# Performance work log

Measured on AMD Instinct MI355X. Metric: run time of the kernel, lower is better.

The kernel has to match this reference:

```python
import jax, jax.numpy as jnp
import numpy as np

HIDDEN = 1024
NUM_EXPERTS = 8
TOP_K = 2
CAPACITY_FACTOR = 1.5
B, S = 2, 2048


def setup_inputs() -> dict:
    key = jax.random.key(0)
    k0, k1, k2 = jax.random.split(key, 3)
    sc1 = 1.0 / np.sqrt(HIDDEN)
    return {
        "hidden_states": jax.random.normal(k0, (B, S, HIDDEN), dtype=jnp.float32),
        "w1": jax.random.uniform(k1, (HIDDEN, HIDDEN), jnp.float32, -sc1, sc1),
        "b1": jnp.zeros((HIDDEN,), jnp.float32),
        "w2": jax.random.uniform(k2, (NUM_EXPERTS, HIDDEN), jnp.float32, -sc1, sc1),
        "b2": jnp.zeros((NUM_EXPERTS,), jnp.float32),
    }


def reference(hidden_states, w1, b1, w2, b2):
    bsz, seq, hid = hidden_states.shape
    # router MLP: Linear -> ReLU -> Linear
    h = jax.nn.relu(jnp.einsum("bsh,oh->bso", hidden_states, w1) + b1)
    router_logits = jnp.einsum("bsh,eh->bse", h, w2) + b2  # [B,S,E]
    router_probs = jax.nn.softmax(router_logits, axis=-1)

    top_k_probs, top_k_indices = jax.lax.top_k(router_probs, TOP_K)  # [B,S,K]
    top_k_probs = top_k_probs / jnp.sum(top_k_probs, axis=-1, keepdims=True)

    capacity = int(bsz * seq * CAPACITY_FACTOR * TOP_K / NUM_EXPERTS)  # static

    # Original writes ONLY capacity slot 0 for each selected expert.
    onehot = jax.nn.one_hot(top_k_indices, NUM_EXPERTS, dtype=router_probs.dtype)  # [B,S,K,E]
    slot0_dispatch = jnp.sum(onehot, axis=-2)                      # [B,S,E] (top-k experts distinct)
    slot0_combine = jnp.einsum("bske,bsk->bse", onehot, top_k_probs)

    dispatch_tensor = jnp.zeros((bsz, seq, NUM_EXPERTS, capacity), router_probs.dtype)
    dispatch_tensor = dispatch_tensor.at[..., 0].set(slot0_dispatch)
    combine_tensor = jnp.zeros((bsz, seq, NUM_EXPERTS, capacity), router_probs.dtype)
    combine_tensor = combine_tensor.at[..., 0].set(slot0_combine)

    router_prob_per_expert = jnp.mean(router_probs, axis=(0, 1))  # [E]
    aux_loss = jnp.sum(router_prob_per_expert * jnp.log(router_prob_per_expert * NUM_EXPERTS + 1e-9))
    return dispatch_tensor, combine_tensor, router_probs, aux_loss
```

## Files before the change

kernel.cpp:

```cpp
#include <hip/hip_runtime.h>
#include <hip/hip_bf16.h>
#include <math.h>

#define HID  1024
#define NEXP 8
#define CAP  1536
#define NTOK 4096

#define DISP_OFF 0ull
#define COMB_OFF 50331648ull
#define RP_OFF   100663296ull
#define AUX_OFF  100696064ull

typedef float f32x4 __attribute__((ext_vector_type(4)));
typedef short s16x8 __attribute__((ext_vector_type(8)));
typedef unsigned short u16;

#define PART_F 524288
#define OXH_F  526400
#define OXM_F  2623552
#define OWH_F  4720704
#define OWM_F  5244992

__device__ __forceinline__ void cvt8(const float4 v0, const float4 v1, s16x8& hi, s16x8& mi)
{
    float f[8] = {v0.x, v0.y, v0.z, v0.w, v1.x, v1.y, v1.z, v1.w};
#pragma unroll
    for (int i = 0; i < 8; ++i) {
        __hip_bfloat16 h = __float2bfloat16(f[i]);
        float fh = __bfloat162float(h);
        __hip_bfloat16 m = __float2bfloat16(f[i] - fh);
        hi[i] = (short)__builtin_bit_cast(unsigned short, h);
        mi[i] = (short)__builtin_bit_cast(unsigned short, m);
    }
}

__device__ __forceinline__ void gload16(const void* g, void* l)
{
    __builtin_amdgcn_global_load_lds(
        (const __attribute__((address_space(1))) unsigned int*)g,
        (__attribute__((address_space(3))) unsigned int*)l, 16, 0, 0);
}

__global__ __launch_bounds__(256) void prep_kernel(
    const float* __restrict__ X, const float* __restrict__ W1, float* __restrict__ ws)
{
    const int g = blockIdx.x * 256 + threadIdx.x;
    const float* src;
    u16 *dh, *dm;
    int idx;
    if (g < 524288) { src = X;  dh = (u16*)(ws + OXH_F); dm = (u16*)(ws + OXM_F); idx = g; }
    else            { src = W1; dh = (u16*)(ws + OWH_F); dm = (u16*)(ws + OWM_F); idx = g - 524288; }
    float4 v0 = *(const float4*)(src + (size_t)idx * 8);
    float4 v1 = *(const float4*)(src + (size_t)idx * 8 + 4);
    s16x8 hi, mi;
    cvt8(v0, v1, hi, mi);
    *(s16x8*)(dh + (size_t)idx * 8) = hi;
    *(s16x8*)(dm + (size_t)idx * 8) = mi;
}

__global__ void fused_kernel(
    const float* __restrict__ B1, const float* __restrict__ W2,
    float* __restrict__ ws, float* __restrict__ out)
{
    __shared__ s16x8 L[2][4][128][4];
    const int tid = threadIdx.x, bid = blockIdx.x;

    if (bid >= 256) {
        const int zid = bid - 256;
        f32x4* p = (f32x4*)out + (size_t)zid * 98304 + tid;
        f32x4 z = (f32x4)0.0f;
#pragma unroll 8
        for (int i = 0; i < 384; ++i) { __builtin_nontemporal_store(z, p); p += 256; }
        return;
    }

    const int n0 = (bid & 7) * 128;
    const int m0 = (bid >> 3) * 128;
    const int wave = tid >> 6, lane = tid & 63;
    const int wr = wave >> 1, wc = wave & 1;
    const int fr = lane & 15, fk = lane >> 4;

    const u16* XH = (const u16*)(ws + OXH_F);
    const u16* XM = (const u16*)(ws + OXM_F);
    const u16* WH = (const u16*)(ws + OWH_F);
    const u16* WM = (const u16*)(ws + OWM_F);

    const int sr4 = lane >> 2;
    const int cg  = (lane & 3) ^ (sr4 & 3);
    const u16* sb = (wave & 2)
        ? (((wave & 1) ? WM : WH) + (size_t)(n0 + sr4) * HID + cg * 8)
        : (((wave & 1) ? XM : XH) + (size_t)(m0 + sr4) * HID + cg * 8);
    char* db = (char*)&L[0][wave][0][0];

    f32x4 acc[4][4];
#pragma unroll
    for (int i = 0; i < 4; ++i)
#pragma unroll
        for (int j = 0; j < 4; ++j) acc[i][j] = (f32x4)0.0f;

#pragma unroll
    for (int i = 0; i < 8; ++i)
        gload16(sb + (size_t)i * 16 * HID, db + i * 1024);
    __syncthreads();

    for (int kk = 0; kk < 32; ++kk) {
        const int b = kk & 1;
        if (kk + 1 < 32) {
            const u16* s = sb + (kk + 1) * 32;
            char* d = db + (b ^ 1) * 32768;
#pragma unroll
            for (int i = 0; i < 8; ++i)
                gload16(s + (size_t)i * 16 * HID, d + i * 1024);
        }

        const s16x8 (*LAh)[4] = L[b][0];
        const s16x8 (*LAm)[4] = L[b][1];
        const s16x8 (*LBh)[4] = L[b][2];
        const s16x8 (*LBm)[4] = L[b][3];
        const int sl = fk ^ (fr & 3);
        s16x8 bh[4], bm[4];
#pragma unroll
        for (int j = 0; j < 4; ++j) {
            const int rb = wc * 64 + j * 16 + fr;
            bh[j] = LBh[rb][sl];
            bm[j] = LBm[rb][sl];
        }
#pragma unroll
        for (int i = 0; i < 4; ++i) {
            const int ra = wr * 64 + i * 16 + fr;
            s16x8 ah = LAh[ra][sl];
            s16x8 am = LAm[ra][sl];
#pragma unroll
            for (int j = 0; j < 4; ++j) {
                acc[i][j] = __builtin_amdgcn_mfma_f32_16x16x32_bf16(ah, bh[j], acc[i][j], 0, 0, 0);
                acc[i][j] = __builtin_amdgcn_mfma_f32_16x16x32_bf16(ah, bm[j], acc[i][j], 0, 0, 0);
                acc[i][j] = __builtin_amdgcn_mfma_f32_16x16x32_bf16(am, bh[j], acc[i][j], 0, 0, 0);
            }
        }
        __syncthreads();
    }

    const int colbase = n0 + wc * 64 + fr;
#pragma unroll
    for (int j = 0; j < 4; ++j) {
        const float bj = B1[colbase + j * 16];
#pragma unroll
        for (int i = 0; i < 4; ++i)
#pragma unroll
            for (int r = 0; r < 4; ++r)
                acc[i][j][r] = fmaxf(acc[i][j][r] + bj, 0.f);
    }

    const int slice = (bid & 7) * 2 + wc;
    float* pbase = ws + ((size_t)slice * NTOK + (m0 + wr * 64 + fk * 4)) * NEXP;
#pragma unroll
    for (int e = 0; e < 8; ++e) {
        const float w20 = W2[e * HID + colbase];
        const float w21 = W2[e * HID + colbase + 16];
        const float w22 = W2[e * HID + colbase + 32];
        const float w23 = W2[e * HID + colbase + 48];
        float pe[16];
#pragma unroll
        for (int i = 0; i < 4; ++i)
#pragma unroll
            for (int r = 0; r < 4; ++r)
                pe[i * 4 + r] = acc[i][0][r] * w20 + acc[i][1][r] * w21 +
                                acc[i][2][r] * w22 + acc[i][3][r] * w23;
#pragma unroll
        for (int m = 1; m <= 8; m <<= 1)
#pragma unroll
            for (int q = 0; q < 16; ++q)
                pe[q] += __shfl_xor(pe[q], m, 64);
        if (fr == 0) {
#pragma unroll
            for (int i = 0; i < 4; ++i)
#pragma unroll
                for (int r = 0; r < 4; ++r)
                    pbase[(size_t)(i * 16 + r) * NEXP + e] = pe[i * 4 + r];
        }
    }
}

__global__ __launch_bounds__(256) void router2_kernel(
    const float* __restrict__ ws, const float* __restrict__ B2, float* __restrict__ out)
{
    const int t = blockIdx.x * 256 + threadIdx.x;
    float lg[8];
#pragma unroll
    for (int e = 0; e < 8; ++e) lg[e] = 0.f;
#pragma unroll
    for (int s = 0; s < 16; ++s) {
        const float* p = ws + ((size_t)s * NTOK + t) * NEXP;
        f32x4 v0 = *(const f32x4*)p;
        f32x4 v1 = *(const f32x4*)(p + 4);
        lg[0] += v0.x; lg[1] += v0.y; lg[2] += v0.z; lg[3] += v0.w;
        lg[4] += v1.x; lg[5] += v1.y; lg[6] += v1.z; lg[7] += v1.w;
    }
#pragma unroll
    for (int e = 0; e < 8; ++e) lg[e] += B2[e];

    float mx = lg[0];
#pragma unroll
    for (int e = 1; e < 8; ++e) mx = fmaxf(mx, lg[e]);
    float pr[8], s = 0.f;
#pragma unroll
    for (int e = 0; e < 8; ++e) { pr[e] = expf(lg[e] - mx); s += pr[e]; }
    const float inv = 1.f / s;
#pragma unroll
    for (int e = 0; e < 8; ++e) pr[e] *= inv;

    int e1 = 0; float p1 = pr[0];
#pragma unroll
    for (int e = 1; e < 8; ++e) if (pr[e] > p1) { p1 = pr[e]; e1 = e; }
    int e2 = -1; float p2 = -1.f;
#pragma unroll
    for (int e = 0; e < 8; ++e) if (e != e1 && pr[e] > p2) { p2 = pr[e]; e2 = e; }

    const float invs = 1.f / (p1 + p2);
    float* rp = out + RP_OFF + (size_t)t * NEXP;
    f32x4 o0 = {pr[0], pr[1], pr[2], pr[3]};
    f32x4 o1 = {pr[4], pr[5], pr[6], pr[7]};
    *(f32x4*)rp = o0; *(f32x4*)(rp + 4) = o1;

    const size_t base = (size_t)t * NEXP;
    out[DISP_OFF + (base + e1) * CAP] = 1.0f;
    out[DISP_OFF + (base + e2) * CAP] = 1.0f;
    out[COMB_OFF + (base + e1) * CAP] = p1 * invs;
    out[COMB_OFF + (base + e2) * CAP] = p2 * invs;
}

__global__ __launch_bounds__(256) void aux_kernel(float* __restrict__ out)
{
    __shared__ float sm[NEXP][257];
    const int tid = threadIdx.x;
    float s[NEXP];
#pragma unroll
    for (int e = 0; e < 8; ++e) s[e] = 0.f;
    const float* rp = out + RP_OFF;
    for (int t = tid; t < NTOK; t += 256) {
        f32x4 v0 = *(const f32x4*)&rp[(size_t)t * NEXP];
        f32x4 v1 = *(const f32x4*)&rp[(size_t)t * NEXP + 4];
        s[0] += v0.x; s[1] += v0.y; s[2] += v0.z; s[3] += v0.w;
        s[4] += v1.x; s[5] += v1.y; s[6] += v1.z; s[7] += v1.w;
    }
#pragma unroll
    for (int e = 0; e < 8; ++e) sm[e][tid] = s[e];
    __syncthreads();
    for (int st = 128; st > 0; st >>= 1) {
        if (tid < st) {
#pragma unroll
            for (int e = 0; e < 8; ++e) sm[e][tid] += sm[e][tid + st];
        }
        __syncthreads();
    }
    if (tid == 0) {
        float loss = 0.f;
#pragma unroll
        for (int e = 0; e < 8; ++e) {
            float m = sm[e][0] * (1.0f / NTOK);
            loss += m * logf(m * (float)NEXP + 1e-9f);
        }
        out[AUX_OFF] = loss;
    }
}

extern "C" void kernel_launch(void* const* d_in, const int* in_sizes, int n_in,
                              void* d_out, int out_size, void* d_ws, size_t ws_size,
                              hipStream_t stream)
{
    const float* x  = (const float*)d_in[0];
    const float* w1 = (const float*)d_in[1];
    const float* b1 = (const float*)d_in[2];
    const float* w2 = (const float*)d_in[3];
    const float* b2 = (const float*)d_in[4];
    float* out = (float*)d_out;
    float* ws  = (float*)d_ws;

    prep_kernel<<<2560, 256, 0, stream>>>(x, w1, ws);
    fused_kernel<<<512, 256, 0, stream>>>(b1, w2, ws, out);
    router2_kernel<<<16, 256, 0, stream>>>(ws, b2, out);
    aux_kernel<<<1, 256, 0, stream>>>(out);
}
```

Measured before the change: 442.7 us.

## Interleave output zero-fill stores into GEMM k-loop with 512-thread blocks

Removes the separate zero-fill blocks and has each GEMM block issue nontemporal zero stores for its slice of the output inside every k-iteration, overlapping the large memory-bound fill with MFMA compute. Blocks grow to 512 threads (8 waves), each wave owning a 32x64 sub-tile, so per-wave accumulator registers halve and each wave loads half as many LDS rows. The cost is more store traffic competing with the global-to-LDS loads, and only 256 blocks in the grid.

```diff
diff --git a/kernel.cpp b/kernel.cpp
--- a/kernel.cpp
+++ b/kernel.cpp
@@ -59,21 +59,12 @@
     *(s16x8*)(dm + (size_t)idx * 8) = mi;
 }
 
-__global__ void fused_kernel(
+__global__ __launch_bounds__(512) void fused_kernel(
     const float* __restrict__ B1, const float* __restrict__ W2,
     float* __restrict__ ws, float* __restrict__ out)
 {
     __shared__ s16x8 L[2][4][128][4];
     const int tid = threadIdx.x, bid = blockIdx.x;
-
-    if (bid >= 256) {
-        const int zid = bid - 256;
-        f32x4* p = (f32x4*)out + (size_t)zid * 98304 + tid;
-        f32x4 z = (f32x4)0.0f;
-#pragma unroll 8
-        for (int i = 0; i < 384; ++i) { __builtin_nontemporal_store(z, p); p += 256; }
-        return;
-    }
 
     const int n0 = (bid & 7) * 128;
     const int m0 = (bid >> 3) * 128;
@@ -86,32 +77,41 @@
     const u16* WH = (const u16*)(ws + OWH_F);
     const u16* WM = (const u16*)(ws + OWM_F);
 
+    f32x4* zp = (f32x4*)out + (size_t)bid * 98304 + tid;
+    const f32x4 zv = (f32x4)0.0f;
+
+    const int st = wave >> 1, hf = wave & 1;
     const int sr4 = lane >> 2;
     const int cg  = (lane & 3) ^ (sr4 & 3);
-    const u16* sb = (wave & 2)
-        ? (((wave & 1) ? WM : WH) + (size_t)(n0 + sr4) * HID + cg * 8)
-        : (((wave & 1) ? XM : XH) + (size_t)(m0 + sr4) * HID + cg * 8);
-    char* db = (char*)&L[0][wave][0][0];
-
-    f32x4 acc[4][4];
+    const u16* sb = (st >= 2)
+        ? (((st == 3) ? WM : WH) + (size_t)(n0 + hf * 64 + sr4) * HID + cg * 8)
+        : (((st == 1) ? XM : XH) + (size_t)(m0 + hf * 64 + sr4) * HID + cg * 8);
+    char* db0 = (char*)&L[0][st][0][0] + hf * 4096;
+
+    f32x4 acc[2][4];
+#pragma unroll
+    for (int i = 0; i < 2; ++i)
+#pragma unroll
+        for (int j = 0; j < 4; ++j) acc[i][j] = (f32x4)0.0f;
+
 #pragma unroll
     for (int i = 0; i < 4; ++i)
-#pragma unroll
-        for (int j = 0; j < 4; ++j) acc[i][j] = (f32x4)0.0f;
-
-#pragma unroll
-    for (int i = 0; i < 8; ++i)
-        gload16(sb + (size_t)i * 16 * HID, db + i * 1024);
+        gload16(sb + (size_t)i * 16 * HID, db0 + i * 1024);
     __syncthreads();
 
     for (int kk = 0; kk < 32; ++kk) {
         const int b = kk & 1;
         if (kk + 1 < 32) {
-            const u16* s = sb + (kk + 1) * 32;
-            char* d = db + (b ^ 1) * 32768;
-#pragma unroll
-            for (int i = 0; i < 8; ++i)
+            const u16* s = sb + (size_t)(kk + 1) * 32;
+            char* d = db0 + (b ^ 1) * 32768;
+#pragma unroll
+            for (int i = 0; i < 4; ++i)
                 gload16(s + (size_t)i * 16 * HID, d + i * 1024);
+        }
+#pragma unroll
+        for (int i2 = 0; i2 < 6; ++i2) {
+            __builtin_nontemporal_store(zv, zp);
+            zp += 512;
         }
 
         const s16x8 (*LAh)[4] = L[b][0];
@@ -127,8 +127,8 @@
             bm[j] = LBm[rb][sl];
         }
 #pragma unroll
-        for (int i = 0; i < 4; ++i) {
-            const int ra = wr * 64 + i * 16 + fr;
+        for (int i = 0; i < 2; ++i) {
+            const int ra = wr * 32 + i * 16 + fr;
             s16x8 ah = LAh[ra][sl];
             s16x8 am = LAm[ra][sl];
 #pragma unroll
@@ -146,23 +146,23 @@
     for (int j = 0; j < 4; ++j) {
         const float bj = B1[colbase + j * 16];
 #pragma unroll
-        for (int i = 0; i < 4; ++i)
+        for (int i = 0; i < 2; ++i)
 #pragma unroll
             for (int r = 0; r < 4; ++r)
                 acc[i][j][r] = fmaxf(acc[i][j][r] + bj, 0.f);
     }
 
     const int slice = (bid & 7) * 2 + wc;
-    float* pbase = ws + ((size_t)slice * NTOK + (m0 + wr * 64 + fk * 4)) * NEXP;
+    float* pbase = ws + ((size_t)slice * NTOK + (m0 + wr * 32 + fk * 4)) * NEXP;
 #pragma unroll
     for (int e = 0; e < 8; ++e) {
         const float w20 = W2[e * HID + colbase];
         const float w21 = W2[e * HID + colbase + 16];
         const float w22 = W2[e * HID + colbase + 32];
         const float w23 = W2[e * HID + colbase + 48];
-        float pe[16];
-#pragma unroll
-        for (int i = 0; i < 4; ++i)
+        float pe[8];
+#pragma unroll
+        for (int i = 0; i < 2; ++i)
 #pragma unroll
             for (int r = 0; r < 4; ++r)
                 pe[i * 4 + r] = acc[i][0][r] * w20 + acc[i][1][r] * w21 +
@@ -170,11 +170,11 @@
 #pragma unroll
         for (int m = 1; m <= 8; m <<= 1)
 #pragma unroll
-            for (int q = 0; q < 16; ++q)
+            for (int q = 0; q < 8; ++q)
                 pe[q] += __shfl_xor(pe[q], m, 64);
         if (fr == 0) {
 #pragma unroll
-            for (int i = 0; i < 4; ++i)
+            for (int i = 0; i < 2; ++i)
 #pragma unroll
                 for (int r = 0; r < 4; ++r)
                     pbase[(size_t)(i * 16 + r) * NEXP + e] = pe[i * 4 + r];
@@ -278,7 +278,7 @@
     float* ws  = (float*)d_ws;
 
     prep_kernel<<<2560, 256, 0, stream>>>(x, w1, ws);
-    fused_kernel<<<512, 256, 0, stream>>>(b1, w2, ws, out);
+    fused_kernel<<<256, 512, 0, stream>>>(b1, w2, ws, out);
     router2_kernel<<<16, 256, 0, stream>>>(ws, b2, out);
     aux_kernel<<<1, 256, 0, stream>>>(out);
 }
```

Result: no change. 443.0 us (+0.1%).
